# Kernel optimization log

Measured on AMD Instinct MI355X. Metric: run time of the kernel, lower is better.

Reference implementation:

```python
import jax, jax.numpy as jnp
import numpy as np

B, N, D = 8, 128, 512

def setup_inputs() -> dict:
    key = jax.random.key(0)
    ks = jax.random.split(key, 8)
    def lin_w(k, fan_in, shape):
        bound = 1.0 / np.sqrt(fan_in)
        return jax.random.uniform(k, shape, jnp.float32, -bound, bound)
    return {
        "features": jax.random.normal(ks[0], (B, N, D), jnp.float32),
        "positions": jax.random.uniform(ks[1], (B, N, 2), jnp.float32),
        "W1": lin_w(ks[2], 2 * D + 2, (2 * D + 2, D)),
        "b1": lin_w(ks[3], 2 * D + 2, (D,)),
        "W2": lin_w(ks[4], D, (D, D // 2)),
        "b2": lin_w(ks[5], D, (D // 2,)),
        "W3": lin_w(ks[6], D // 2, (D // 2, 4)),
        "b3": lin_w(ks[7], D // 2, (4,)),
    }

def reference(features, positions, W1, b1, W2, b2, W3, b3):
    d = features.shape[-1]
    # Split first linear: concat([f1, f2, pos_diff]) @ W1 == f1@W1a + f2@W1b + pos_diff@W1c
    W1a, W1b, W1c = W1[:d], W1[d:2 * d], W1[2 * d:]
    h1 = jnp.einsum("bnd,dk->bnk", features, W1a)          # broadcast over axis 2 (j)
    h2 = jnp.einsum("bmd,dk->bmk", features, W1b)          # broadcast over axis 1 (i)
    pos_diff = positions[:, :, None, :] - positions[:, None, :, :]  # [B,N,N,2]
    h = h1[:, :, None, :] + h2[:, None, :, :] + jnp.einsum("bnmp,pk->bnmk", pos_diff, W1c) + b1
    h = jax.nn.relu(h)
    h = jax.nn.relu(jnp.einsum("bnmk,kl->bnml", h, W2) + b2)
    return jnp.einsum("bnml,lo->bnmo", h, W3) + b3          # [B,N,N,4]
```

## Files before the change

kernel.cpp:

```cpp
#include <hip/hip_runtime.h>
#include <hip/hip_bf16.h>

typedef unsigned short u16;
typedef unsigned int u32;
typedef __attribute__((ext_vector_type(8))) _Float16 f16x8;
typedef __attribute__((ext_vector_type(2))) _Float16 f16x2;
typedef __attribute__((ext_vector_type(4))) float floatx4;

__device__ __forceinline__ u16 f2h(float f){
    union{_Float16 h; u16 u;}v; v.h = (_Float16)f; return v.u;
}
__device__ __forceinline__ u32 pkh(float a, float b){
    return (u32)f2h(a) | ((u32)f2h(b) << 16);
}

#define DD 512
#define NTOK 128

__global__ __launch_bounds__(512) void prep_k(
    const float* __restrict__ features, const float* __restrict__ W1,
    const float* __restrict__ W2, const float* __restrict__ b1,
    const float* __restrict__ positions,
    u16* __restrict__ Hf1b, u16* __restrict__ Hf2, u16* __restrict__ W2T)
{
    const int z = blockIdx.z;
    const int tid = threadIdx.x;

    if (z == 2) {
        __shared__ u16 tile[32][33];
        const int tx = tid & 31, ty = tid >> 5;
        const int r0 = blockIdx.x * 32, c0 = blockIdx.y * 32;
#pragma unroll
        for (int i = 0; i < 2; ++i) {
            int r = ty + i * 16;
            tile[r][tx] = f2h(W2[(size_t)(r0 + r) * 256 + (c0 + tx)]);
        }
        __syncthreads();
#pragma unroll
        for (int i = 0; i < 2; ++i) {
            int c = ty + i * 16;
            W2T[(size_t)(c0 + c) * 512 + (r0 + tx)] = tile[tx][c];
        }
        return;
    }

    const int bM = blockIdx.x, bN = blockIdx.y;
    u16* outp = z ? Hf2 : Hf1b;
    __shared__ __align__(16) u16 At[64 * 64];
    __shared__ __align__(16) u16 Btl[64 * 64];
    const int wid = tid >> 6, lane = tid & 63, lrow = lane & 15, quad = lane >> 4;
    const int wm = wid >> 1, wn = wid & 1;

    floatx4 acc[2];
    acc[0] = (floatx4)(0.0f); acc[1] = (floatx4)(0.0f);

    const int m = tid >> 3, seg = tid & 7, sw = m & 7;
    const int kr = tid >> 3, csB = tid & 7;

    for (int kc = 0; kc < 8; ++kc) {
        const int k0 = kc * 64;
        {
            const float4* src = (const float4*)(features + (size_t)(bM * 64 + m) * DD + k0 + seg * 8);
            float4 f0 = src[0], f1 = src[1];
            *(uint4*)(At + m * 64 + ((seg ^ sw) << 3)) =
                make_uint4(pkh(f0.x, f0.y), pkh(f0.z, f0.w), pkh(f1.x, f1.y), pkh(f1.z, f1.w));
        }
        {
            const float4* src = (const float4*)(W1 + (size_t)(z * 512 + k0 + kr) * DD + bN * 64 + csB * 8);
            float4 g0 = src[0], g1 = src[1];
            float f[8] = { g0.x, g0.y, g0.z, g0.w, g1.x, g1.y, g1.z, g1.w };
            const int chunkB = (kr >> 3), offB = kr & 7;
#pragma unroll
            for (int i = 0; i < 8; ++i) {
                int c = csB * 8 + i;
                Btl[c * 64 + ((chunkB ^ i) << 3) + offB] = f2h(f[i]);
            }
        }
        __syncthreads();
#pragma unroll
        for (int ks = 0; ks < 2; ++ks) {
            const int ch = ks * 4 + quad;
            int r = wm * 16 + lrow;
            f16x8 afr = *(const f16x8*)(At + r * 64 + ((ch ^ (r & 7)) << 3));
#pragma unroll
            for (int j = 0; j < 2; ++j) {
                int c = wn * 32 + j * 16 + lrow;
                f16x8 bfr = *(const f16x8*)(Btl + c * 64 + ((ch ^ (c & 7)) << 3));
                acc[j] = __builtin_amdgcn_mfma_f32_16x16x32_f16(afr, bfr, acc[j], 0, 0, 0);
            }
        }
        __syncthreads();
    }
#pragma unroll
    for (int j = 0; j < 2; ++j) {
        int col = bN * 64 + wn * 32 + j * 16 + lrow;
        float bb  = z ? 0.0f : b1[col];
        float c0v = W1[(size_t)1024 * DD + col];
        float c1v = W1[(size_t)1025 * DD + col];
        float sgn = z ? -1.0f : 1.0f;
#pragma unroll
        for (int r = 0; r < 4; ++r) {
            int row = bM * 64 + wm * 16 + quad * 4 + r;
            float pxr = positions[(size_t)row * 2 + 0];
            float pyr = positions[(size_t)row * 2 + 1];
            outp[(size_t)row * DD + col] =
                f2h(acc[j][r] + bb + sgn * (pxr * c0v + pyr * c1v));
        }
    }
}

__global__ __launch_bounds__(512) void fused_main(
    const u16* __restrict__ Hf1b, const u16* __restrict__ Hf2,
    const u16* __restrict__ W2T, const float* __restrict__ b2,
    const float* __restrict__ W3, const float* __restrict__ b3,
    float* __restrict__ out)
{
    const int b = blockIdx.x, n = blockIdx.y;
    const int tid = threadIdx.x;
    const int base_bn = b * NTOK + n;
    const int wid = tid >> 6, lane = tid & 63, lrow = lane & 15, quad = lane >> 4;

    __shared__ __align__(16) u16 s1h[DD];
    __shared__ __align__(16) char mbuf[49152];
    u16* Atile = (u16*)mbuf;
    u16* Btile = (u16*)(mbuf + 16384);
    u16* gh    = (u16*)mbuf;
    u16* w3t   = (u16*)(mbuf + 34816);

    {
        int k = tid;
        s1h[k] = Hf1b[(size_t)base_bn * DD + k];
    }
    const int mrow = tid >> 2, seg = tid & 3, swA = mrow & 7;
    const int csrc = lane >> 3, wsrc = lane & 7;
    const u16* bsrc_lane = W2T + csrc * DD + ((wsrc ^ csrc) << 3);
    __syncthreads();

    const int wm = wid >> 2, wn = wid & 3;
    floatx4 acc[4][4];
#pragma unroll
    for (int i = 0; i < 4; ++i)
#pragma unroll
        for (int j = 0; j < 4; ++j) acc[i][j] = (floatx4)(0.0f);

    const u16* hf2p = Hf2 + (size_t)(b * NTOK + mrow) * DD;

    const f16x2 zh = {(_Float16)0.0f, (_Float16)0.0f};
    auto hp2 = [&](u32 h, u32 s) -> u32 {
        union { u32 u; f16x2 v; } H, S, O;
        H.u = h; S.u = s;
        O.v = __builtin_elementwise_max(H.v + S.v, zh);
        return O.u;
    };

    for (int kc = 0; kc < 8; ++kc) {
        const int k0 = kc * 64;
#pragma unroll
        for (int q = 0; q < 4; ++q) {
            const int slot = wid * 4 + q;
            __builtin_amdgcn_global_load_lds(
                (const __attribute__((address_space(1))) u32*)(bsrc_lane + slot * 8 * DD + k0),
                (__attribute__((address_space(3))) u32*)(Btile + slot * 512), 16, 0, 0);
        }

        const int kb = k0 + seg * 16;
        {
            uint4 hv  = *(const uint4*)(hf2p + kb);
            uint4 hw  = *(const uint4*)(hf2p + kb + 8);
            uint4 sv  = *(const uint4*)(s1h + kb);
            uint4 sw2 = *(const uint4*)(s1h + kb + 8);
            uint4 o0 = make_uint4(hp2(hv.x, sv.x), hp2(hv.y, sv.y),
                                  hp2(hv.z, sv.z), hp2(hv.w, sv.w));
            uint4 o1 = make_uint4(hp2(hw.x, sw2.x), hp2(hw.y, sw2.y),
                                  hp2(hw.z, sw2.z), hp2(hw.w, sw2.w));
            *(uint4*)(Atile + mrow * 64 + (((seg * 2    ) ^ swA) << 3)) = o0;
            *(uint4*)(Atile + mrow * 64 + (((seg * 2 + 1) ^ swA) << 3)) = o1;
        }
        __syncthreads();
#pragma unroll
        for (int ks = 0; ks < 2; ++ks) {
            const int ch = ks * 4 + quad;
            f16x8 afr[4], bfr[4];
#pragma unroll
            for (int i = 0; i < 4; ++i) {
                int r = wm * 64 + i * 16 + lrow;
                afr[i] = *(const f16x8*)(Atile + r * 64 + ((ch ^ (r & 7)) << 3));
            }
#pragma unroll
            for (int j = 0; j < 4; ++j) {
                int c = wn * 64 + j * 16 + lrow;
                bfr[j] = *(const f16x8*)(Btile + c * 64 + ((ch ^ (c & 7)) << 3));
            }
#pragma unroll
            for (int i = 0; i < 4; ++i)
#pragma unroll
                for (int j = 0; j < 4; ++j)
                    acc[i][j] = __builtin_amdgcn_mfma_f32_16x16x32_f16(afr[i], bfr[j], acc[i][j], 0, 0, 0);
        }
        __syncthreads();
    }

    {
        int c = tid & 15, kb2 = tid >> 4;
        int k0w = kb2 * 8;
        u32 wv[4];
#pragma unroll
        for (int p = 0; p < 4; ++p) {
            int ka = k0w + p * 2;
            u16 va = (c < 4) ? f2h(W3[ka * 4 + c])       : (u16)0;
            u16 vb = (c < 4) ? f2h(W3[(ka + 1) * 4 + c]) : (u16)0;
            wv[p] = (u32)va | ((u32)vb << 16);
        }
        *(uint2*)(w3t + c * 264 + k0w)     = make_uint2(wv[0], wv[1]);
        *(uint2*)(w3t + c * 264 + k0w + 4) = make_uint2(wv[2], wv[3]);
    }

    float b2v[4];
#pragma unroll
    for (int j = 0; j < 4; ++j) b2v[j] = b2[wn * 64 + j * 16 + lrow];

    const int smrow = wid * 16;
    floatx4 acc3 = (floatx4)(0.0f);
#pragma unroll
    for (int half = 0; half < 2; ++half) {
        __syncthreads();
        if ((wn >> 1) == half) {
#pragma unroll
            for (int i = 0; i < 4; ++i)
#pragma unroll
                for (int j = 0; j < 4; ++j)
#pragma unroll
                    for (int r = 0; r < 4; ++r) {
                        int row = wm * 64 + i * 16 + quad * 4 + r;
                        int col = (wn & 1) * 64 + j * 16 + lrow;
                        gh[row * 136 + col] = f2h(fmaxf(acc[i][j][r] + b2v[j], 0.0f));
                    }
        }
        __syncthreads();
#pragma unroll
        for (int ks = 0; ks < 4; ++ks) {
            f16x8 gfrag = *(const f16x8*)(gh + (smrow + lrow) * 136 + ks * 32 + quad * 8);
            f16x8 wfrag = *(const f16x8*)(w3t + lrow * 264 + half * 128 + ks * 32 + quad * 8);
            acc3 = __builtin_amdgcn_mfma_f32_16x16x32_f16(gfrag, wfrag, acc3, 0, 0, 0);
        }
    }
    if (lrow < 4) {
        float bo = b3[lrow];
#pragma unroll
        for (int r = 0; r < 4; ++r) {
            int row = smrow + quad * 4 + r;
            out[(size_t)base_bn * 512 + row * 4 + lrow] = acc3[r] + bo;
        }
    }
}

extern "C" void kernel_launch(void* const* d_in, const int* in_sizes, int n_in,
                              void* d_out, int out_size, void* d_ws, size_t ws_size,
                              hipStream_t stream)
{
    const float* features  = (const float*)d_in[0];
    const float* positions = (const float*)d_in[1];
    const float* W1 = (const float*)d_in[2];
    const float* b1 = (const float*)d_in[3];
    const float* W2 = (const float*)d_in[4];
    const float* b2 = (const float*)d_in[5];
    const float* W3 = (const float*)d_in[6];
    const float* b3 = (const float*)d_in[7];
    float* out = (float*)d_out;

    char* ws = (char*)d_ws;
    u16* W2T  = (u16*)(ws);
    u16* Hf1b = (u16*)(ws + 262144);
    u16* Hf2  = (u16*)(ws + 1310720);

    prep_k<<<dim3(16, 8, 3), 512, 0, stream>>>(features, W1, W2, b1, positions,
                                               Hf1b, Hf2, W2T);
    fused_main<<<dim3(8, 128), 512, 0, stream>>>(Hf1b, Hf2, W2T, b2, W3, b3, out);
}
```

Measured before the change: 115.5 us.

## Double-buffer W2 tile DMA and build A fragments directly in registers

New measurement: 171.2 us. 48.3% more time.

```diff
diff --git a/kernel.cpp b/kernel.cpp
--- a/kernel.cpp
+++ b/kernel.cpp
@@ -121,19 +121,31 @@
     const int wid = tid >> 6, lane = tid & 63, lrow = lane & 15, quad = lane >> 4;
 
     __shared__ __align__(16) u16 s1h[DD];
-    __shared__ __align__(16) char mbuf[49152];
-    u16* Atile = (u16*)mbuf;
-    u16* Btile = (u16*)(mbuf + 16384);
+    __shared__ __align__(16) char mbuf[65536];
+    u16* Btile = (u16*)mbuf;
     u16* gh    = (u16*)mbuf;
     u16* w3t   = (u16*)(mbuf + 34816);
+
+    const int csrc = lane >> 3, wsrc = lane & 7;
+    const u16* bsrc_lane = W2T + csrc * DD + ((wsrc ^ csrc) << 3);
+
+    auto BDMA = [&](int kc) {
+        const int qoff = (kc & 1) * 16384;
+#pragma unroll
+        for (int q = 0; q < 4; ++q) {
+            const int slot = wid * 4 + q;
+            __builtin_amdgcn_global_load_lds(
+                (const __attribute__((address_space(1))) u32*)(bsrc_lane + slot * 8 * DD + kc * 64),
+                (__attribute__((address_space(3))) u32*)(Btile + qoff + slot * 512), 16, 0, 0);
+        }
+    };
+
+    BDMA(0);
 
     {
         int k = tid;
         s1h[k] = Hf1b[(size_t)base_bn * DD + k];
     }
-    const int mrow = tid >> 2, seg = tid & 3, swA = mrow & 7;
-    const int csrc = lane >> 3, wsrc = lane & 7;
-    const u16* bsrc_lane = W2T + csrc * DD + ((wsrc ^ csrc) << 3);
     __syncthreads();
 
     const int wm = wid >> 2, wn = wid & 3;
@@ -143,7 +155,7 @@
 #pragma unroll
         for (int j = 0; j < 4; ++j) acc[i][j] = (floatx4)(0.0f);
 
-    const u16* hf2p = Hf2 + (size_t)(b * NTOK + mrow) * DD;
+    const u16* hfbase = Hf2 + ((size_t)(b * NTOK) + wm * 64 + lrow) * DD + quad * 8;
 
     const f16x2 zh = {(_Float16)0.0f, (_Float16)0.0f};
     auto hp2 = [&](u32 h, u32 s) -> u32 {
@@ -154,51 +166,51 @@
     };
 
     for (int kc = 0; kc < 8; ++kc) {
-        const int k0 = kc * 64;
-#pragma unroll
-        for (int q = 0; q < 4; ++q) {
-            const int slot = wid * 4 + q;
-            __builtin_amdgcn_global_load_lds(
-                (const __attribute__((address_space(1))) u32*)(bsrc_lane + slot * 8 * DD + k0),
-                (__attribute__((address_space(3))) u32*)(Btile + slot * 512), 16, 0, 0);
-        }
-
-        const int kb = k0 + seg * 16;
-        {
-            uint4 hv  = *(const uint4*)(hf2p + kb);
-            uint4 hw  = *(const uint4*)(hf2p + kb + 8);
-            uint4 sv  = *(const uint4*)(s1h + kb);
-            uint4 sw2 = *(const uint4*)(s1h + kb + 8);
-            uint4 o0 = make_uint4(hp2(hv.x, sv.x), hp2(hv.y, sv.y),
-                                  hp2(hv.z, sv.z), hp2(hv.w, sv.w));
-            uint4 o1 = make_uint4(hp2(hw.x, sw2.x), hp2(hw.y, sw2.y),
-                                  hp2(hw.z, sw2.z), hp2(hw.w, sw2.w));
-            *(uint4*)(Atile + mrow * 64 + (((seg * 2    ) ^ swA) << 3)) = o0;
-            *(uint4*)(Atile + mrow * 64 + (((seg * 2 + 1) ^ swA) << 3)) = o1;
-        }
-        __syncthreads();
+        uint4 rA[4][2];
+#pragma unroll
+        for (int i = 0; i < 4; ++i)
+#pragma unroll
+            for (int ks = 0; ks < 2; ++ks)
+                rA[i][ks] = *(const uint4*)(hfbase + (size_t)i * 16 * DD + kc * 64 + ks * 32);
+        uint4 sfr[2];
+#pragma unroll
+        for (int ks = 0; ks < 2; ++ks)
+            sfr[ks] = *(const uint4*)(s1h + kc * 64 + ks * 32 + quad * 8);
+#pragma unroll
+        for (int i = 0; i < 4; ++i)
+#pragma unroll
+            for (int ks = 0; ks < 2; ++ks) {
+                rA[i][ks].x = hp2(rA[i][ks].x, sfr[ks].x);
+                rA[i][ks].y = hp2(rA[i][ks].y, sfr[ks].y);
+                rA[i][ks].z = hp2(rA[i][ks].z, sfr[ks].z);
+                rA[i][ks].w = hp2(rA[i][ks].w, sfr[ks].w);
+            }
+
+        __syncthreads();
+
+        if (kc < 7) BDMA(kc + 1);
+
+        const int qs = (kc & 1) * 16384;
 #pragma unroll
         for (int ks = 0; ks < 2; ++ks) {
             const int ch = ks * 4 + quad;
-            f16x8 afr[4], bfr[4];
-#pragma unroll
-            for (int i = 0; i < 4; ++i) {
-                int r = wm * 64 + i * 16 + lrow;
-                afr[i] = *(const f16x8*)(Atile + r * 64 + ((ch ^ (r & 7)) << 3));
-            }
+            f16x8 bfr[4];
 #pragma unroll
             for (int j = 0; j < 4; ++j) {
                 int c = wn * 64 + j * 16 + lrow;
-                bfr[j] = *(const f16x8*)(Btile + c * 64 + ((ch ^ (c & 7)) << 3));
-            }
-#pragma unroll
-            for (int i = 0; i < 4; ++i)
+                bfr[j] = *(const f16x8*)(Btile + qs + c * 64 + ((ch ^ (c & 7)) << 3));
+            }
+#pragma unroll
+            for (int i = 0; i < 4; ++i) {
+                union { uint4 u; f16x8 v; } afr;
+                afr.u = rA[i][ks];
 #pragma unroll
                 for (int j = 0; j < 4; ++j)
-                    acc[i][j] = __builtin_amdgcn_mfma_f32_16x16x32_f16(afr[i], bfr[j], acc[i][j], 0, 0, 0);
-        }
-        __syncthreads();
-    }
+                    acc[i][j] = __builtin_amdgcn_mfma_f32_16x16x32_f16(afr.v, bfr[j], acc[i][j], 0, 0, 0);
+            }
+        }
+    }
+    __syncthreads();
 
     {
         int c = tid & 15, kb2 = tid >> 4;
```

## Use 256-thread blocks with 64x128 per-warp tiles in fused main kernel

Applied to the files above, without the earlier changes.

Result: slower. 153.7 us (+33.2%).

```diff
diff --git a/kernel.cpp b/kernel.cpp
--- a/kernel.cpp
+++ b/kernel.cpp
@@ -109,7 +109,7 @@
     }
 }
 
-__global__ __launch_bounds__(512) void fused_main(
+__global__ __launch_bounds__(256) void fused_main(
     const u16* __restrict__ Hf1b, const u16* __restrict__ Hf2,
     const u16* __restrict__ W2T, const float* __restrict__ b2,
     const float* __restrict__ W3, const float* __restrict__ b3,
@@ -128,20 +128,20 @@
     u16* w3t   = (u16*)(mbuf + 34816);
 
     {
-        int k = tid;
-        s1h[k] = Hf1b[(size_t)base_bn * DD + k];
-    }
-    const int mrow = tid >> 2, seg = tid & 3, swA = mrow & 7;
+        s1h[tid]       = Hf1b[(size_t)base_bn * DD + tid];
+        s1h[tid + 256] = Hf1b[(size_t)base_bn * DD + tid + 256];
+    }
+    const int mrow = tid >> 1, seg2 = tid & 1, swA = mrow & 7;
     const int csrc = lane >> 3, wsrc = lane & 7;
     const u16* bsrc_lane = W2T + csrc * DD + ((wsrc ^ csrc) << 3);
     __syncthreads();
 
-    const int wm = wid >> 2, wn = wid & 3;
-    floatx4 acc[4][4];
+    const int wm = wid >> 1, wn = wid & 1;
+    floatx4 acc[4][8];
 #pragma unroll
     for (int i = 0; i < 4; ++i)
 #pragma unroll
-        for (int j = 0; j < 4; ++j) acc[i][j] = (floatx4)(0.0f);
+        for (int j = 0; j < 8; ++j) acc[i][j] = (floatx4)(0.0f);
 
     const u16* hf2p = Hf2 + (size_t)(b * NTOK + mrow) * DD;
 
@@ -156,52 +156,51 @@
     for (int kc = 0; kc < 8; ++kc) {
         const int k0 = kc * 64;
 #pragma unroll
-        for (int q = 0; q < 4; ++q) {
-            const int slot = wid * 4 + q;
+        for (int q = 0; q < 8; ++q) {
+            const int slot = wid * 8 + q;
             __builtin_amdgcn_global_load_lds(
                 (const __attribute__((address_space(1))) u32*)(bsrc_lane + slot * 8 * DD + k0),
                 (__attribute__((address_space(3))) u32*)(Btile + slot * 512), 16, 0, 0);
         }
 
-        const int kb = k0 + seg * 16;
+        const int kb = k0 + seg2 * 32;
         {
-            uint4 hv  = *(const uint4*)(hf2p + kb);
-            uint4 hw  = *(const uint4*)(hf2p + kb + 8);
-            uint4 sv  = *(const uint4*)(s1h + kb);
-            uint4 sw2 = *(const uint4*)(s1h + kb + 8);
-            uint4 o0 = make_uint4(hp2(hv.x, sv.x), hp2(hv.y, sv.y),
-                                  hp2(hv.z, sv.z), hp2(hv.w, sv.w));
-            uint4 o1 = make_uint4(hp2(hw.x, sw2.x), hp2(hw.y, sw2.y),
-                                  hp2(hw.z, sw2.z), hp2(hw.w, sw2.w));
-            *(uint4*)(Atile + mrow * 64 + (((seg * 2    ) ^ swA) << 3)) = o0;
-            *(uint4*)(Atile + mrow * 64 + (((seg * 2 + 1) ^ swA) << 3)) = o1;
+#pragma unroll
+            for (int t = 0; t < 4; ++t) {
+                uint4 hv = *(const uint4*)(hf2p + kb + t * 8);
+                uint4 sv = *(const uint4*)(s1h + kb + t * 8);
+                uint4 o = make_uint4(hp2(hv.x, sv.x), hp2(hv.y, sv.y),
+                                     hp2(hv.z, sv.z), hp2(hv.w, sv.w));
+                *(uint4*)(Atile + mrow * 64 + (((seg2 * 4 + t) ^ swA) << 3)) = o;
+            }
         }
         __syncthreads();
 #pragma unroll
         for (int ks = 0; ks < 2; ++ks) {
             const int ch = ks * 4 + quad;
-            f16x8 afr[4], bfr[4];
+            f16x8 afr[4], bfr[8];
 #pragma unroll
             for (int i = 0; i < 4; ++i) {
                 int r = wm * 64 + i * 16 + lrow;
                 afr[i] = *(const f16x8*)(Atile + r * 64 + ((ch ^ (r & 7)) << 3));
             }
 #pragma unroll
-            for (int j = 0; j < 4; ++j) {
-                int c = wn * 64 + j * 16 + lrow;
+            for (int j = 0; j < 8; ++j) {
+                int c = wn * 128 + j * 16 + lrow;
                 bfr[j] = *(const f16x8*)(Btile + c * 64 + ((ch ^ (c & 7)) << 3));
             }
 #pragma unroll
             for (int i = 0; i < 4; ++i)
 #pragma unroll
-                for (int j = 0; j < 4; ++j)
+                for (int j = 0; j < 8; ++j)
                     acc[i][j] = __builtin_amdgcn_mfma_f32_16x16x32_f16(afr[i], bfr[j], acc[i][j], 0, 0, 0);
         }
         __syncthreads();
     }
 
-    {
-        int c = tid & 15, kb2 = tid >> 4;
+#pragma unroll
+    for (int it = 0; it < 2; ++it) {
+        int c = tid & 15, kb2 = (tid >> 4) + it * 16;
         int k0w = kb2 * 8;
         u32 wv[4];
 #pragma unroll
@@ -215,42 +214,48 @@
         *(uint2*)(w3t + c * 264 + k0w + 4) = make_uint2(wv[2], wv[3]);
     }
 
-    float b2v[4];
-#pragma unroll
-    for (int j = 0; j < 4; ++j) b2v[j] = b2[wn * 64 + j * 16 + lrow];
-
-    const int smrow = wid * 16;
-    floatx4 acc3 = (floatx4)(0.0f);
+    float b2v[8];
+#pragma unroll
+    for (int j = 0; j < 8; ++j) b2v[j] = b2[wn * 128 + j * 16 + lrow];
+
+    floatx4 acc3[2];
+    acc3[0] = (floatx4)(0.0f); acc3[1] = (floatx4)(0.0f);
 #pragma unroll
     for (int half = 0; half < 2; ++half) {
         __syncthreads();
-        if ((wn >> 1) == half) {
+        if (wn == half) {
 #pragma unroll
             for (int i = 0; i < 4; ++i)
 #pragma unroll
-                for (int j = 0; j < 4; ++j)
+                for (int j = 0; j < 8; ++j)
 #pragma unroll
                     for (int r = 0; r < 4; ++r) {
                         int row = wm * 64 + i * 16 + quad * 4 + r;
-                        int col = (wn & 1) * 64 + j * 16 + lrow;
+                        int col = j * 16 + lrow;
                         gh[row * 136 + col] = f2h(fmaxf(acc[i][j][r] + b2v[j], 0.0f));
                     }
         }
         __syncthreads();
 #pragma unroll
-        for (int ks = 0; ks < 4; ++ks) {
-            f16x8 gfrag = *(const f16x8*)(gh + (smrow + lrow) * 136 + ks * 32 + quad * 8);
-            f16x8 wfrag = *(const f16x8*)(w3t + lrow * 264 + half * 128 + ks * 32 + quad * 8);
-            acc3 = __builtin_amdgcn_mfma_f32_16x16x32_f16(gfrag, wfrag, acc3, 0, 0, 0);
+        for (int g = 0; g < 2; ++g) {
+            const int grow = wid * 32 + g * 16;
+#pragma unroll
+            for (int ks = 0; ks < 4; ++ks) {
+                f16x8 gfrag = *(const f16x8*)(gh + (grow + lrow) * 136 + ks * 32 + quad * 8);
+                f16x8 wfrag = *(const f16x8*)(w3t + lrow * 264 + half * 128 + ks * 32 + quad * 8);
+                acc3[g] = __builtin_amdgcn_mfma_f32_16x16x32_f16(gfrag, wfrag, acc3[g], 0, 0, 0);
+            }
         }
     }
     if (lrow < 4) {
         float bo = b3[lrow];
 #pragma unroll
-        for (int r = 0; r < 4; ++r) {
-            int row = smrow + quad * 4 + r;
-            out[(size_t)base_bn * 512 + row * 4 + lrow] = acc3[r] + bo;
-        }
+        for (int g = 0; g < 2; ++g)
+#pragma unroll
+            for (int r = 0; r < 4; ++r) {
+                int row = wid * 32 + g * 16 + quad * 4 + r;
+                out[(size_t)base_bn * 512 + row * 4 + lrow] = acc3[g][r] + bo;
+            }
     }
 }
 
@@ -275,5 +280,5 @@
 
     prep_k<<<dim3(16, 8, 3), 512, 0, stream>>>(features, W1, W2, b1, positions,
                                                Hf1b, Hf2, W2T);
-    fused_main<<<dim3(8, 128), 512, 0, stream>>>(Hf1b, Hf2, W2T, b2, W3, b3, out);
-}
+    fused_main<<<dim3(8, 128), 256, 0, stream>>>(Hf1b, Hf2, W2T, b2, W3, b3, out);
+}
```
